# Performance work log

Hardware: AMD Instinct MI355X
Metric: run time of the kernel (lower is better)

## Reference

```python
import jax, jax.numpy as jnp
import numpy as np
import math

B, S, H, D = 8, 2048, 1024, 64  # batch, seq_len, hidden_dim, head_size

def setup_inputs() -> dict:
    key = jax.random.key(0)
    ks = jax.random.split(key, 7)
    lim = 1.0 / math.sqrt(H)  # torch Linear default init bound
    return {
        "x":  jax.random.normal(ks[0], (B, S, H), dtype=jnp.float32),
        "Wq": jax.random.uniform(ks[1], (H, D), jnp.float32, -lim, lim),
        "bq": jax.random.uniform(ks[2], (D,),   jnp.float32, -lim, lim),
        "Wk": jax.random.uniform(ks[3], (H, D), jnp.float32, -lim, lim),
        "bk": jax.random.uniform(ks[4], (D,),   jnp.float32, -lim, lim),
        "Wv": jax.random.uniform(ks[5], (H, D), jnp.float32, -lim, lim),
        "bv": jax.random.uniform(ks[6], (D,),   jnp.float32, -lim, lim),
    }

def reference(x, Wq, bq, Wk, bk, Wv, bv):
    # x: [B, S, H]
    q = x @ Wq + bq          # [B, S, D]
    k = x @ Wk + bk          # [B, S, D]
    v = x @ Wv + bv          # [B, S, D]
    scores = jnp.einsum("bsd,btd->bst", q, k)       # [B, S, S]
    causal = jnp.tril(jnp.ones((S, S), dtype=bool))
    scores = jnp.where(causal, scores, -jnp.inf)
    # NOTE: original module (faithfully) applies softmax FIRST, then divides
    # by sqrt(hidden_dim) -- it does NOT scale logits before softmax.
    weight = jax.nn.softmax(scores, axis=-1) / jnp.sqrt(jnp.float32(x.shape[-1]))
    # dropout p=0.0 -> identity
    return jnp.einsum("bst,btd->bsd", weight, v)     # [B, S, D]
```

## Files before the change

### kernel.cpp

```cpp
#include <hip/hip_runtime.h>


typedef float     f32x4 __attribute__((ext_vector_type(4)));
typedef _Float16  f16x8 __attribute__((ext_vector_type(8)));
typedef _Float16  f16x4 __attribute__((ext_vector_type(4)));

__device__ __forceinline__ float wave_max16(float v) {
  #pragma unroll
  for (int off = 1; off < 16; off <<= 1) v = fmaxf(v, __shfl_xor(v, off, 64));
  return v;
}
__device__ __forceinline__ float wave_sum16(float v) {
  #pragma unroll
  for (int off = 1; off < 16; off <<= 1) v += __shfl_xor(v, off, 64);
  return v;
}

__global__ __launch_bounds__(256) void wt_prep(const float* __restrict__ Wq,
                                               const float* __restrict__ Wk,
                                               const float* __restrict__ Wv,
                                               _Float16* __restrict__ WtF) {
  const int w  = blockIdx.x >> 4;
  const int kt = blockIdx.x & 15;
  const float* src = (w == 0) ? Wq : (w == 1 ? Wk : Wv);
  __shared__ _Float16 ls[64][72];
  const int t = threadIdx.x;
  {
    int rr = t >> 4;
    int c4 = (t & 15) * 4;
    #pragma unroll
    for (int ri = 0; ri < 4; ++ri) {
      int k = rr + ri * 16;
      f32x4 f = *(const f32x4*)&src[(size_t)(kt * 64 + k) * 64 + c4];
      #pragma unroll
      for (int j = 0; j < 4; ++j) ls[k][c4 + j] = (_Float16)f[j];
    }
  }
  __syncthreads();
  const int lane = t & 63, l16 = lane & 15, quad = lane >> 4;
  #pragma unroll
  for (int h = 0; h < 2; ++h) {
    int fid     = h * 4 + (t >> 6);
    int kstep_l = fid >> 2;
    int ntl     = fid & 3;
    int nt      = w * 4 + ntl;
    int kstep   = kt * 2 + kstep_l;
    f16x8 o;
    #pragma unroll
    for (int j = 0; j < 8; ++j) o[j] = ls[kstep_l * 32 + quad * 8 + j][ntl * 16 + l16];
    *(f16x8*)&WtF[((size_t)(kstep * 12 + nt) * 64 + lane) * 8] = o;
  }
}

__global__ __launch_bounds__(512, 4) void qkv_gemm(const float* __restrict__ x,
                                                   const _Float16* __restrict__ WtF,
                                                   const float* __restrict__ bq,
                                                   const float* __restrict__ bk,
                                                   const float* __restrict__ bv,
                                                   _Float16* __restrict__ qo,
                                                   _Float16* __restrict__ ko,
                                                   _Float16* __restrict__ vt) {
  __shared__ _Float16 xs[32 * 1024];
  const int tid  = threadIdx.x;
  const int wave = tid >> 6, lane = tid & 63;
  const int l16  = lane & 15, quad = lane >> 4;
  const int mhalf = wave >> 2;
  const int ngrp  = wave & 3;
  const int m0    = blockIdx.x * 32;

  {
    int row   = tid >> 4;
    int cbase = (tid & 15) * 4;
    const float* xrow = x + (size_t)(m0 + row) * 1024;
    int key = row & 7;
    #pragma unroll
    for (int j = 0; j < 16; ++j) {
      int col = cbase + j * 64;
      f32x4 f = *(const f32x4*)&xrow[col];
      f16x4 hh;
      #pragma unroll
      for (int e = 0; e < 4; ++e) hh[e] = (_Float16)f[e];
      int g   = col >> 3;
      int sub = col & 7;
      *(f16x4*)&xs[(size_t)row * 1024 + (size_t)((g ^ key) << 3) + sub] = hh;
    }
  }
  __syncthreads();

  f32x4 acc0 = (f32x4){0.f,0.f,0.f,0.f};
  f32x4 acc1 = (f32x4){0.f,0.f,0.f,0.f};
  f32x4 acc2 = (f32x4){0.f,0.f,0.f,0.f};

  const int arow = mhalf * 16 + l16;
  const _Float16* abase = xs + (size_t)arow * 1024;
  const int akey = arow & 7;
  const _Float16* wbase = WtF + ((size_t)(ngrp * 3) * 64 + lane) * 8;

  #pragma unroll 4
  for (int kstep = 0; kstep < 32; ++kstep) {
    f16x8 a = *(const f16x8*)(abase + (((kstep * 4 + quad) ^ akey) << 3));
    const _Float16* wk = wbase + (size_t)kstep * (12 * 64 * 8);
    f16x8 b0 = *(const f16x8*)(wk);
    f16x8 b1 = *(const f16x8*)(wk + 512);
    f16x8 b2 = *(const f16x8*)(wk + 1024);
    acc0 = __builtin_amdgcn_mfma_f32_16x16x32_f16(a, b0, acc0, 0, 0, 0);
    acc1 = __builtin_amdgcn_mfma_f32_16x16x32_f16(a, b1, acc1, 0, 0, 0);
    acc2 = __builtin_amdgcn_mfma_f32_16x16x32_f16(a, b2, acc2, 0, 0, 0);
  }

  f32x4 accs[3] = {acc0, acc1, acc2};
  #pragma unroll
  for (int i = 0; i < 3; ++i) {
    int nt  = ngrp * 3 + i;
    int col = nt * 16 + l16;
    float bias = (nt < 4) ? bq[col] : (nt < 8) ? bk[col - 64] : bv[col - 128];
    #pragma unroll
    for (int r = 0; r < 4; ++r) {
      int m = m0 + mhalf * 16 + quad * 4 + r;
      _Float16 hv = (_Float16)(accs[i][r] + bias);
      if (nt < 4)      qo[(size_t)m * 64 + col] = hv;
      else if (nt < 8) ko[(size_t)m * 64 + (col - 64)] = hv;
      else {
        int b = m >> 11, s = m & 2047;
        vt[((size_t)b * 64 + (col - 128)) * 2048 + s] = hv;
      }
    }
  }
}

__global__ __launch_bounds__(256) void attn(const _Float16* __restrict__ q,
                                            const _Float16* __restrict__ k,
                                            const _Float16* __restrict__ vt,
                                            float* __restrict__ out) {
  const int blk  = blockIdx.x;
  const int qt   = 127 - (blk >> 3);
  const int b    = blk & 7;
  const int tid  = threadIdx.x;
  const int wave = tid >> 6, lane = tid & 63;
  const int l16  = lane & 15, quad = lane >> 4;
  const int q0   = qt * 16;

  __shared__ _Float16 P[4][16][72];
  __shared__ float    ob[4][16][66];
  __shared__ float    mlb[4][2][16];

  const _Float16* qb = q  + (size_t)b * 2048 * 64;
  const _Float16* kb = k  + (size_t)b * 2048 * 64;
  const _Float16* vb = vt + (size_t)b * 64 * 2048;

  f16x8 qf0 = *(const f16x8*)&qb[(q0 + l16) * 64 + quad * 8];
  f16x8 qf1 = *(const f16x8*)&qb[(q0 + l16) * 64 + 32 + quad * 8];

  f32x4 o[4];
  #pragma unroll
  for (int i = 0; i < 4; ++i) o[i] = (f32x4){0.f, 0.f, 0.f, 0.f};
  float mrow[4] = {-1e30f, -1e30f, -1e30f, -1e30f};
  float lrow[4] = {0.f, 0.f, 0.f, 0.f};
  const float L2E = 1.44269504088896340736f;

  const int kvend = q0 + 16;
  for (int kv0 = wave * 64; kv0 < kvend; kv0 += 256) {
    f32x4 sc[4];
    #pragma unroll
    for (int t = 0; t < 4; ++t) {
      int kvc = kv0 + t * 16;
      f32x4 c = (f32x4){0.f, 0.f, 0.f, 0.f};
      if (kvc < kvend) {
        f16x8 kf0 = *(const f16x8*)&kb[(kvc + l16) * 64 + quad * 8];
        f16x8 kf1 = *(const f16x8*)&kb[(kvc + l16) * 64 + 32 + quad * 8];
        c = __builtin_amdgcn_mfma_f32_16x16x32_f16(qf0, kf0, c, 0, 0, 0);
        c = __builtin_amdgcn_mfma_f32_16x16x32_f16(qf1, kf1, c, 0, 0, 0);
      }
      sc[t] = c;
    }
    if (kv0 + 63 > q0) {
      #pragma unroll
      for (int t = 0; t < 4; ++t) {
        int skv = kv0 + t * 16 + l16;
        #pragma unroll
        for (int r = 0; r < 4; ++r) {
          int sq = q0 + quad * 4 + r;
          if (skv > sq) sc[t][r] = -1e30f;
        }
      }
    }
    float alpha[4];
    #pragma unroll
    for (int r = 0; r < 4; ++r) {
      float mx = fmaxf(fmaxf(sc[0][r], sc[1][r]), fmaxf(sc[2][r], sc[3][r]));
      mx = wave_max16(mx);
      float mnew = fmaxf(mrow[r], mx);
      alpha[r] = exp2f((mrow[r] - mnew) * L2E);
      mrow[r] = mnew;
    }
    #pragma unroll
    for (int t = 0; t < 4; ++t)
      #pragma unroll
      for (int r = 0; r < 4; ++r)
        sc[t][r] = exp2f((sc[t][r] - mrow[r]) * L2E);
    #pragma unroll
    for (int r = 0; r < 4; ++r) {
      float s = sc[0][r] + sc[1][r] + sc[2][r] + sc[3][r];
      s = wave_sum16(s);
      lrow[r] = lrow[r] * alpha[r] + s;
      #pragma unroll
      for (int dt = 0; dt < 4; ++dt) o[dt][r] *= alpha[r];
    }
    #pragma unroll
    for (int t = 0; t < 4; ++t)
      #pragma unroll
      for (int r = 0; r < 4; ++r)
        P[wave][quad * 4 + r][t * 16 + l16] = (_Float16)sc[t][r];
    asm volatile("s_waitcnt lgkmcnt(0)" ::: "memory");
    f16x8 p0 = *(const f16x8*)&P[wave][l16][quad * 8];
    f16x8 p1 = *(const f16x8*)&P[wave][l16][32 + quad * 8];
    #pragma unroll
    for (int dt = 0; dt < 4; ++dt) {
      f16x8 v0 = *(const f16x8*)&vb[(size_t)(dt * 16 + l16) * 2048 + kv0 + quad * 8];
      f16x8 v1 = *(const f16x8*)&vb[(size_t)(dt * 16 + l16) * 2048 + kv0 + 32 + quad * 8];
      o[dt] = __builtin_amdgcn_mfma_f32_16x16x32_f16(p0, v0, o[dt], 0, 0, 0);
      o[dt] = __builtin_amdgcn_mfma_f32_16x16x32_f16(p1, v1, o[dt], 0, 0, 0);
    }
  }

  #pragma unroll
  for (int dt = 0; dt < 4; ++dt)
    #pragma unroll
    for (int r = 0; r < 4; ++r)
      ob[wave][quad * 4 + r][dt * 16 + l16] = o[dt][r];
  if (l16 == 0) {
    #pragma unroll
    for (int r = 0; r < 4; ++r) {
      mlb[wave][0][quad * 4 + r] = mrow[r];
      mlb[wave][1][quad * 4 + r] = lrow[r];
    }
  }
  __syncthreads();

  {
    int row = tid >> 4;
    int c0  = (tid & 15) * 4;
    float m0 = mlb[0][0][row], m1 = mlb[1][0][row];
    float m2 = mlb[2][0][row], m3 = mlb[3][0][row];
    float M  = fmaxf(fmaxf(m0, m1), fmaxf(m2, m3));
    float w0 = exp2f((m0 - M) * L2E), w1 = exp2f((m1 - M) * L2E);
    float w2 = exp2f((m2 - M) * L2E), w3 = exp2f((m3 - M) * L2E);
    float L  = w0 * mlb[0][1][row] + w1 * mlb[1][1][row]
             + w2 * mlb[2][1][row] + w3 * mlb[3][1][row];
    float inv = 1.0f / (L * 32.0f);
    f32x4 res;
    #pragma unroll
    for (int j = 0; j < 4; ++j)
      res[j] = (w0 * ob[0][row][c0 + j] + w1 * ob[1][row][c0 + j]
              + w2 * ob[2][row][c0 + j] + w3 * ob[3][row][c0 + j]) * inv;
    *(f32x4*)&out[((size_t)b * 2048 + q0 + row) * 64 + c0] = res;
  }
}

extern "C" void kernel_launch(void* const* d_in, const int* in_sizes, int n_in,
                              void* d_out, int out_size, void* d_ws, size_t ws_size,
                              hipStream_t stream) {
  const float* x  = (const float*)d_in[0];
  const float* Wq = (const float*)d_in[1];
  const float* bq = (const float*)d_in[2];
  const float* Wk = (const float*)d_in[3];
  const float* bk = (const float*)d_in[4];
  const float* Wv = (const float*)d_in[5];
  const float* bv = (const float*)d_in[6];
  float* out = (float*)d_out;

  _Float16* WtF = (_Float16*)d_ws;
  _Float16* qo  = WtF + 192 * 1024;
  _Float16* ko  = qo + 16384 * 64;
  _Float16* vt  = ko + 16384 * 64;

  hipLaunchKernelGGL(wt_prep,  dim3(48),   dim3(256), 0, stream, Wq, Wk, Wv, WtF);
  hipLaunchKernelGGL(qkv_gemm, dim3(512),  dim3(512), 0, stream, x, WtF, bq, bk, bv, qo, ko, vt);
  hipLaunchKernelGGL(attn,     dim3(1024), dim3(256), 0, stream, qo, ko, vt, out);
}
```

Measured before the change: 156.6 us.

## Transpose MFMA operands so each lane owns one query row, widen KV chunk to 128

The attention kernel swaps the MFMA operand order so the score and output tiles come out transposed, with each lane holding a single query row. Row max and row sum then take two cross-lane shuffles instead of four per row, and the P and output stores become vector writes. Each wave now handles 128 KV positions per iteration instead of 64, halving the loop trips and online-softmax rescales, and launch bounds request 4 blocks per CU. In exchange it uses more registers and LDS per wave and wastes more work on the partial last chunk of short causal rows.

```diff
diff --git a/kernel.cpp b/kernel.cpp
--- a/kernel.cpp
+++ b/kernel.cpp
@@ -4,17 +4,6 @@
 typedef float     f32x4 __attribute__((ext_vector_type(4)));
 typedef _Float16  f16x8 __attribute__((ext_vector_type(8)));
 typedef _Float16  f16x4 __attribute__((ext_vector_type(4)));
-
-__device__ __forceinline__ float wave_max16(float v) {
-  #pragma unroll
-  for (int off = 1; off < 16; off <<= 1) v = fmaxf(v, __shfl_xor(v, off, 64));
-  return v;
-}
-__device__ __forceinline__ float wave_sum16(float v) {
-  #pragma unroll
-  for (int off = 1; off < 16; off <<= 1) v += __shfl_xor(v, off, 64);
-  return v;
-}
 
 __global__ __launch_bounds__(256) void wt_prep(const float* __restrict__ Wq,
                                                const float* __restrict__ Wk,
@@ -128,10 +117,10 @@
   }
 }
 
-__global__ __launch_bounds__(256) void attn(const _Float16* __restrict__ q,
-                                            const _Float16* __restrict__ k,
-                                            const _Float16* __restrict__ vt,
-                                            float* __restrict__ out) {
+__global__ __launch_bounds__(256, 4) void attn(const _Float16* __restrict__ q,
+                                               const _Float16* __restrict__ k,
+                                               const _Float16* __restrict__ vt,
+                                               float* __restrict__ out) {
   const int blk  = blockIdx.x;
   const int qt   = 127 - (blk >> 3);
   const int b    = blk & 7;
@@ -140,8 +129,8 @@
   const int l16  = lane & 15, quad = lane >> 4;
   const int q0   = qt * 16;
 
-  __shared__ _Float16 P[4][16][72];
-  __shared__ float    ob[4][16][66];
+  __shared__ _Float16 P[4][16][136];
+  __shared__ float    ob[4][16][68];
   __shared__ float    mlb[4][2][16];
 
   const _Float16* qb = q  + (size_t)b * 2048 * 64;
@@ -154,86 +143,87 @@
   f32x4 o[4];
   #pragma unroll
   for (int i = 0; i < 4; ++i) o[i] = (f32x4){0.f, 0.f, 0.f, 0.f};
-  float mrow[4] = {-1e30f, -1e30f, -1e30f, -1e30f};
-  float lrow[4] = {0.f, 0.f, 0.f, 0.f};
+  float m = -1e30f, l = 0.f;
   const float L2E = 1.44269504088896340736f;
-
+  const int qrow  = q0 + l16;
   const int kvend = q0 + 16;
-  for (int kv0 = wave * 64; kv0 < kvend; kv0 += 256) {
-    f32x4 sc[4];
-    #pragma unroll
-    for (int t = 0; t < 4; ++t) {
+
+  for (int kv0 = wave * 128; kv0 < kvend; kv0 += 512) {
+    f32x4 sc[8];
+    #pragma unroll
+    for (int t = 0; t < 8; ++t) {
       int kvc = kv0 + t * 16;
-      f32x4 c = (f32x4){0.f, 0.f, 0.f, 0.f};
+      f32x4 c;
       if (kvc < kvend) {
+        c = (f32x4){0.f, 0.f, 0.f, 0.f};
         f16x8 kf0 = *(const f16x8*)&kb[(kvc + l16) * 64 + quad * 8];
         f16x8 kf1 = *(const f16x8*)&kb[(kvc + l16) * 64 + 32 + quad * 8];
-        c = __builtin_amdgcn_mfma_f32_16x16x32_f16(qf0, kf0, c, 0, 0, 0);
-        c = __builtin_amdgcn_mfma_f32_16x16x32_f16(qf1, kf1, c, 0, 0, 0);
+        c = __builtin_amdgcn_mfma_f32_16x16x32_f16(kf0, qf0, c, 0, 0, 0);
+        c = __builtin_amdgcn_mfma_f32_16x16x32_f16(kf1, qf1, c, 0, 0, 0);
+        if (kvc + 15 > q0) {
+          #pragma unroll
+          for (int r = 0; r < 4; ++r)
+            if (kvc + quad * 4 + r > qrow) c[r] = -1e30f;
+        }
+      } else {
+        c = (f32x4){-1e30f, -1e30f, -1e30f, -1e30f};
       }
       sc[t] = c;
     }
-    if (kv0 + 63 > q0) {
-      #pragma unroll
-      for (int t = 0; t < 4; ++t) {
-        int skv = kv0 + t * 16 + l16;
+
+    float mx = -1e30f;
+    #pragma unroll
+    for (int t = 0; t < 8; ++t)
+      mx = fmaxf(mx, fmaxf(fmaxf(sc[t][0], sc[t][1]), fmaxf(sc[t][2], sc[t][3])));
+    mx = fmaxf(mx, __shfl_xor(mx, 16, 64));
+    mx = fmaxf(mx, __shfl_xor(mx, 32, 64));
+    float mnew  = fmaxf(m, mx);
+    float alpha = exp2f((m - mnew) * L2E);
+    m = mnew;
+
+    float s = 0.f;
+    #pragma unroll
+    for (int t = 0; t < 8; ++t) {
+      #pragma unroll
+      for (int r = 0; r < 4; ++r) sc[t][r] = exp2f((sc[t][r] - m) * L2E);
+      s += (sc[t][0] + sc[t][1]) + (sc[t][2] + sc[t][3]);
+    }
+    s += __shfl_xor(s, 16, 64);
+    s += __shfl_xor(s, 32, 64);
+    l = l * alpha + s;
+    #pragma unroll
+    for (int dt = 0; dt < 4; ++dt)
+      #pragma unroll
+      for (int r = 0; r < 4; ++r) o[dt][r] *= alpha;
+
+    #pragma unroll
+    for (int t = 0; t < 8; ++t) {
+      f16x4 ph;
+      #pragma unroll
+      for (int r = 0; r < 4; ++r) ph[r] = (_Float16)sc[t][r];
+      *(f16x4*)&P[wave][l16][t * 16 + quad * 4] = ph;
+    }
+    asm volatile("s_waitcnt lgkmcnt(0)" ::: "memory");
+
+    #pragma unroll
+    for (int ks = 0; ks < 4; ++ks) {
+      if (kv0 + ks * 32 < kvend) {
+        f16x8 pf = *(const f16x8*)&P[wave][l16][ks * 32 + quad * 8];
         #pragma unroll
-        for (int r = 0; r < 4; ++r) {
-          int sq = q0 + quad * 4 + r;
-          if (skv > sq) sc[t][r] = -1e30f;
+        for (int dt = 0; dt < 4; ++dt) {
+          f16x8 vf = *(const f16x8*)&vb[(size_t)(dt * 16 + l16) * 2048 + kv0 + ks * 32 + quad * 8];
+          o[dt] = __builtin_amdgcn_mfma_f32_16x16x32_f16(vf, pf, o[dt], 0, 0, 0);
         }
       }
     }
-    float alpha[4];
-    #pragma unroll
-    for (int r = 0; r < 4; ++r) {
-      float mx = fmaxf(fmaxf(sc[0][r], sc[1][r]), fmaxf(sc[2][r], sc[3][r]));
-      mx = wave_max16(mx);
-      float mnew = fmaxf(mrow[r], mx);
-      alpha[r] = exp2f((mrow[r] - mnew) * L2E);
-      mrow[r] = mnew;
-    }
-    #pragma unroll
-    for (int t = 0; t < 4; ++t)
-      #pragma unroll
-      for (int r = 0; r < 4; ++r)
-        sc[t][r] = exp2f((sc[t][r] - mrow[r]) * L2E);
-    #pragma unroll
-    for (int r = 0; r < 4; ++r) {
-      float s = sc[0][r] + sc[1][r] + sc[2][r] + sc[3][r];
-      s = wave_sum16(s);
-      lrow[r] = lrow[r] * alpha[r] + s;
-      #pragma unroll
-      for (int dt = 0; dt < 4; ++dt) o[dt][r] *= alpha[r];
-    }
-    #pragma unroll
-    for (int t = 0; t < 4; ++t)
-      #pragma unroll
-      for (int r = 0; r < 4; ++r)
-        P[wave][quad * 4 + r][t * 16 + l16] = (_Float16)sc[t][r];
-    asm volatile("s_waitcnt lgkmcnt(0)" ::: "memory");
-    f16x8 p0 = *(const f16x8*)&P[wave][l16][quad * 8];
-    f16x8 p1 = *(const f16x8*)&P[wave][l16][32 + quad * 8];
-    #pragma unroll
-    for (int dt = 0; dt < 4; ++dt) {
-      f16x8 v0 = *(const f16x8*)&vb[(size_t)(dt * 16 + l16) * 2048 + kv0 + quad * 8];
-      f16x8 v1 = *(const f16x8*)&vb[(size_t)(dt * 16 + l16) * 2048 + kv0 + 32 + quad * 8];
-      o[dt] = __builtin_amdgcn_mfma_f32_16x16x32_f16(p0, v0, o[dt], 0, 0, 0);
-      o[dt] = __builtin_amdgcn_mfma_f32_16x16x32_f16(p1, v1, o[dt], 0, 0, 0);
-    }
   }
 
   #pragma unroll
   for (int dt = 0; dt < 4; ++dt)
-    #pragma unroll
-    for (int r = 0; r < 4; ++r)
-      ob[wave][quad * 4 + r][dt * 16 + l16] = o[dt][r];
-  if (l16 == 0) {
-    #pragma unroll
-    for (int r = 0; r < 4; ++r) {
-      mlb[wave][0][quad * 4 + r] = mrow[r];
-      mlb[wave][1][quad * 4 + r] = lrow[r];
-    }
+    *(f32x4*)&ob[wave][l16][dt * 16 + quad * 4] = o[dt];
+  if (quad == 0) {
+    mlb[wave][0][l16] = m;
+    mlb[wave][1][l16] = l;
   }
   __syncthreads();
 
```

New measurement: 155.4 us. Within noise of the previous version (-0.8%).
